# Kernel tuning notes

Hardware: AMD Instinct MI355X
Metric: run time of the kernel (lower is better)

## Reference

```python
import jax, jax.numpy as jnp
import numpy as np

N_HEAD = 16

def setup_inputs() -> dict:
    key = jax.random.key(0)
    ks = jax.random.split(key, 9)
    B, T, C = 2, 2048, 1024
    s = 0.02
    return {
        "x": jax.random.normal(ks[0], (B, T, C), dtype=jnp.float32),
        "Wk": jax.random.normal(ks[1], (C, C), dtype=jnp.float32) * s,
        "bk": jnp.zeros((C,), dtype=jnp.float32),
        "Wq": jax.random.normal(ks[2], (C, C), dtype=jnp.float32) * s,
        "bq": jnp.zeros((C,), dtype=jnp.float32),
        "Wv": jax.random.normal(ks[3], (C, C), dtype=jnp.float32) * s,
        "bv": jnp.zeros((C,), dtype=jnp.float32),
        "Wp": jax.random.normal(ks[4], (C, C), dtype=jnp.float32) * s,
        "bp": jnp.zeros((C,), dtype=jnp.float32),
    }

def reference(x, Wk, bk, Wq, bq, Wv, bv, Wp, bp):
    B, T, C = x.shape
    H = N_HEAD
    D = C // H
    # projections -> [B, H, T, D]
    def split_heads(y):
        return y.reshape(B, T, H, D).transpose(0, 2, 1, 3)
    k = split_heads(x @ Wk.T + bk)
    q = split_heads(x @ Wq.T + bq)
    v = split_heads(x @ Wv.T + bv)
    scale = 1.0 / jnp.sqrt(jnp.asarray(D, dtype=x.dtype))
    att = jnp.einsum("bhtd,bhsd->bhts", q, k) * scale  # [B,H,T,T]
    causal = jnp.tril(jnp.ones((T, T), dtype=bool))
    att = jnp.where(causal, att, jnp.asarray(-jnp.inf, dtype=att.dtype))
    att = jax.nn.softmax(att, axis=-1)
    y = jnp.einsum("bhts,bhsd->bhtd", att, v)  # [B,H,T,D]
    y = y.transpose(0, 2, 1, 3).reshape(B, T, C)
    return y @ Wp.T + bp
```

## Files before the change

### kernel.cpp

```cpp
#include <hip/hip_runtime.h>
#include <stdint.h>

typedef unsigned short u16;
typedef __attribute__((ext_vector_type(8))) short short8;
typedef __attribute__((ext_vector_type(4))) short short4v;
typedef __attribute__((ext_vector_type(4))) float float4v;

#define NB 2
#define NT 2048
#define NC 1024
#define NH 16
#define ND 64
#define NM (NB*NT)

#if defined(__has_builtin)
#if __has_builtin(__builtin_amdgcn_mfma_f32_16x16x16bf16_1k)
#define MFMA16(a, b, c) __builtin_amdgcn_mfma_f32_16x16x16bf16_1k(a, b, c, 0, 0, 0)
#endif
#endif
#ifndef MFMA16
static __device__ __forceinline__ float4v mfma16_asm(short4v a, short4v b, float4v c) {
  asm volatile("v_mfma_f32_16x16x16_bf16 %0, %1, %2, %0" : "+v"(c) : "v"(a), "v"(b));
  return c;
}
#define MFMA16(a, b, c) mfma16_asm(a, b, c)
#endif

#define WB4 asm volatile("s_waitcnt vmcnt(4)\n\ts_barrier" ::: "memory")
#define WB0 asm volatile("s_waitcnt vmcnt(0)\n\ts_barrier" ::: "memory")
#define BAR_PLAIN asm volatile("s_barrier" ::: "memory")

__device__ __forceinline__ u16 f2bf(float f) {
  union { float f; uint32_t u; } v; v.f = f;
  uint32_t u = v.u;
  u += 0x7fffu + ((u >> 16) & 1u);
  return (u16)(u >> 16);
}
__device__ __forceinline__ float bf2f(u16 u) {
  union { uint32_t u; float f; } v; v.u = ((uint32_t)u) << 16; return v.f;
}

__device__ __forceinline__ short4v pack4bf(float a, float b, float c, float d) {
  union { uint32_t u[2]; short4v s; } r;
  r.u[0] = __builtin_amdgcn_perm(__float_as_uint(b), __float_as_uint(a), 0x07060302u);
  r.u[1] = __builtin_amdgcn_perm(__float_as_uint(d), __float_as_uint(c), 0x07060302u);
  return r.s;
}

__device__ __forceinline__ void gld_lds16(const u16* g, u16* lds) {
  __builtin_amdgcn_global_load_lds(
      (const __attribute__((address_space(1))) uint32_t*)g,
      (__attribute__((address_space(3))) uint32_t*)lds,
      16, 0, 0);
}

__global__ __launch_bounds__(256) void cast_all(
    const float* __restrict__ x,  const float* __restrict__ wk,
    const float* __restrict__ wq, const float* __restrict__ wv,
    const float* __restrict__ wp,
    u16* __restrict__ xb, u16* __restrict__ wkb, u16* __restrict__ wqb,
    u16* __restrict__ wvb, u16* __restrict__ wpb) {
  const int NX = NM * NC / 4;
  const int NW = NC * NC / 4;
  int i = blockIdx.x * 256 + threadIdx.x;
  const float* src; u16* dst; int off;
  if (i < NX)            { src = x;  dst = xb;  off = i; }
  else if (i < NX+NW)    { src = wk; dst = wkb; off = i - NX; }
  else if (i < NX+2*NW)  { src = wq; dst = wqb; off = i - NX - NW; }
  else if (i < NX+3*NW)  { src = wv; dst = wvb; off = i - NX - 2*NW; }
  else if (i < NX+4*NW)  { src = wp; dst = wpb; off = i - NX - 3*NW; }
  else return;
  float4v f = ((const float4v*)src)[off];
  short4v o;
  o.x = (short)f2bf(f.x); o.y = (short)f2bf(f.y);
  o.z = (short)f2bf(f.z); o.w = (short)f2bf(f.w);
  ((short4v*)dst)[off] = o;
}

__device__ __forceinline__ void gemm_tile(
    const u16* __restrict__ A_tile, const u16* __restrict__ W_tile,
    u16* As, u16* Bs, float4v (&acc)[4][4]) {
  const int tid  = threadIdx.x;
  const int wave = tid >> 6, lane = tid & 63;
  const int quad = lane >> 4, l15 = lane & 15;
  const int wm = wave >> 1, wn = wave & 1;
  const int c8 = lane & 7, r8 = lane >> 3;

#pragma unroll
  for (int i = 0; i < 4; i++)
#pragma unroll
    for (int j = 0; j < 4; j++) acc[i][j] = (float4v){0.f, 0.f, 0.f, 0.f};

  for (int k0 = 0; k0 < NC; k0 += 64) {
#pragma unroll
    for (int i = 0; i < 4; i++) {
      int row = wave * 32 + i * 8 + r8;
      int gc  = c8 ^ (row & 7);
      gld_lds16(A_tile + row * NC + k0 + gc * 8, As + (wave * 32 + i * 8) * 64);
      gld_lds16(W_tile + row * NC + k0 + gc * 8, Bs + (wave * 32 + i * 8) * 64);
    }
    __syncthreads();
#pragma unroll
    for (int kk = 0; kk < 2; kk++) {
      short8 af[4], bf[4];
#pragma unroll
      for (int mt = 0; mt < 4; mt++) {
        int row = wm * 64 + mt * 16 + l15;
        int ch  = (kk * 4 + quad) ^ (row & 7);
        af[mt] = *(const short8*)(As + row * 64 + ch * 8);
      }
#pragma unroll
      for (int nt = 0; nt < 4; nt++) {
        int row = wn * 64 + nt * 16 + l15;
        int ch  = (kk * 4 + quad) ^ (row & 7);
        bf[nt] = *(const short8*)(Bs + row * 64 + ch * 8);
      }
#pragma unroll
      for (int mt = 0; mt < 4; mt++)
#pragma unroll
        for (int nt = 0; nt < 4; nt++)
          acc[mt][nt] = __builtin_amdgcn_mfma_f32_16x16x32_bf16(af[mt], bf[nt], acc[mt][nt], 0, 0, 0);
    }
    __syncthreads();
  }
}

__global__ __launch_bounds__(256) void qkv_gemm(
    const u16* __restrict__ xb,
    const u16* __restrict__ wqb, const u16* __restrict__ wkb, const u16* __restrict__ wvb,
    const float* __restrict__ bq, const float* __restrict__ bk, const float* __restrict__ bv,
    u16* __restrict__ Q, u16* __restrict__ K, u16* __restrict__ Vb) {
  __shared__ u16 As[128 * 64];
  __shared__ u16 Bs[128 * 64];
  const int id  = blockIdx.x;
  const int x8  = id & 7;
  const int rr  = id >> 3;
  const int mti = rr & 31;
  const int mat = rr >> 5;
  const int n0  = x8 * 128;
  const int m0  = mti * 128;
  const u16*   W    = (mat == 0) ? wqb : (mat == 1) ? wkb : wvb;
  const float* bias = (mat == 0) ? bq  : (mat == 1) ? bk  : bv;
  u16* dst = (mat == 0) ? Q : (mat == 1) ? K : Vb;
  const float osc = (mat == 0) ? 0.18033688f : 1.0f;

  float4v acc[4][4];
  gemm_tile(xb + m0 * NC, W + n0 * NC, As, Bs, acc);

  const int tid = threadIdx.x, wave = tid >> 6, lane = tid & 63;
  const int quad = lane >> 4, l15 = lane & 15;
  const int wm = wave >> 1, wn = wave & 1;
#pragma unroll
  for (int nt = 0; nt < 4; nt++) {
    int col = n0 + wn * 64 + nt * 16 + l15;
    float bval = bias[col];
#pragma unroll
    for (int mt = 0; mt < 4; mt++) {
      int rowb = m0 + wm * 64 + mt * 16 + quad * 4;
#pragma unroll
      for (int r = 0; r < 4; r++)
        dst[(size_t)(rowb + r) * NC + col] = f2bf((acc[mt][nt][r] + bval) * osc);
    }
  }
}

__global__ __launch_bounds__(256) void vtrans(const u16* __restrict__ V, u16* __restrict__ Vt) {
  __shared__ u16 tl[64 * 64];
  const int tid = threadIdx.x;
  const int bh = blockIdx.y, b = bh >> 4, h = bh & 15;
  const int t0 = blockIdx.x * 64;
#pragma unroll
  for (int it = 0; it < 2; it++) {
    int idx = it * 256 + tid;
    int row = idx >> 3;
    int ch  = idx & 7;
    short8 vv = *(const short8*)(V + (size_t)(b * NT + t0 + row) * NC + h * ND + ch * 8);
    int p   = ((row >> 2) & 3) * 16 + (row >> 4) * 4 + (row & 3);
    int off = ((p >> 3) ^ ch) * 8 + (p & 7);
#pragma unroll
    for (int j = 0; j < 8; j++) tl[(ch * 8 + j) * 64 + off] = (u16)vv[j];
  }
  __syncthreads();
#pragma unroll
  for (int it = 0; it < 2; it++) {
    int idx = it * 256 + tid;
    int d  = idx >> 3;
    int tc = idx & 7;
    short8 o = *(const short8*)(tl + d * 64 + ((tc ^ ((d >> 3) & 7)) << 3));
    *(short8*)(Vt + (size_t)(bh * ND + d) * NT + t0 + tc * 8) = o;
  }
}

__global__ __launch_bounds__(256, 4) void attn(
    const u16* __restrict__ Q, const u16* __restrict__ K,
    const u16* __restrict__ Vt, u16* __restrict__ O,
    u16* __restrict__ Opart, float* __restrict__ Lpart) {
  __shared__ u16 Kc[2][64 * 64];
  __shared__ u16 Vc[2][64 * 64];

  const int tid = threadIdx.x, wave = tid >> 6, lane = tid & 63;
  const int quad = lane >> 4, l15 = lane & 15;
  const int c8 = lane & 7, r8 = lane >> 3;
  const int id = blockIdx.x;
  const int rr = id >> 3;
  const int cls = rr % 30;
  const int bh = (id & 7) + 8 * (rr / 30);
  const int b = bh >> 4, h = bh & 15;

  int tile, k, c_lo, c_hi, sbase;
  if (cls < 6)        { tile = cls; k = 0;
                        c_lo = 0; c_hi = 2 * tile + 1; sbase = -1; }
  else if (cls < 18)  { tile = 6 + ((cls - 6) >> 1); k = (cls - 6) & 1;
                        int Ch = tile + 1;
                        c_lo = k * Ch; c_hi = c_lo + Ch - 1;
                        sbase = (tile - 6) * 2 + k; }
  else                { int d3 = cls - 18; int t3 = d3 / 3; k = d3 - 3 * t3;
                        tile = 12 + t3; int C = 2 * tile + 2;
                        c_lo = (k * C) / 3; c_hi = ((k + 1) * C) / 3 - 1;
                        sbase = 12 + t3 * 3 + k; }
  const bool partial = (sbase >= 0);
  const int qb0 = tile * 128 + wave * 32;

  short8 qf[2][2];
#pragma unroll
  for (int j = 0; j < 2; j++) {
    const u16* qrow = Q + (size_t)(b * NT + qb0 + j * 16 + l15) * NC + h * ND + quad * 8;
    qf[j][0] = *(const short8*)(qrow);
    qf[j][1] = *(const short8*)(qrow + 32);
  }

  float l_c[2] = {0.f, 0.f};
  float4v o_acc[2][4];
#pragma unroll
  for (int j = 0; j < 2; j++)
#pragma unroll
    for (int dt = 0; dt < 4; dt++) o_acc[j][dt] = (float4v){0.f, 0.f, 0.f, 0.f};

  int kOff[2], vOff[2], ldsOff[2];
#pragma unroll
  for (int ii = 0; ii < 2; ii++) {
    int row = wave * 16 + ii * 8 + r8;
    int gc  = c8 ^ (row & 7);
    kOff[ii]   = row * NC + gc * 8;
    vOff[ii]   = row * NT + gc * 8;
    ldsOff[ii] = (wave * 16 + ii * 8) * 64;
  }
  const u16* Kbase = K  + (size_t)b * NT * NC + h * ND;
  const u16* Vbase = Vt + (size_t)bh * ND * NT;

  auto stage = [&](int ci) {
    const int p = (ci - c_lo) & 1;
    const u16* kc = Kbase + (size_t)ci * (64 * NC);
    const u16* vc = Vbase + ci * 64;
#pragma unroll
    for (int ii = 0; ii < 2; ii++) {
      gld_lds16(kc + kOff[ii], Kc[p] + ldsOff[ii]);
      gld_lds16(vc + vOff[ii], Vc[p] + ldsOff[ii]);
    }
  };

  stage(c_lo);
  for (int i = c_lo; i <= c_hi; i++) {
    const int p = (i - c_lo) & 1;
    if (i < c_hi) { stage(i + 1); WB4; } else { WB0; }
    const u16* Ks = Kc[p];
    const u16* Vs = Vc[p];

    short4v pf[2][4];
#pragma unroll
    for (int sub = 0; sub < 4; sub++) {
      float4v a0 = (float4v){0.f, 0.f, 0.f, 0.f};
      float4v a1 = (float4v){0.f, 0.f, 0.f, 0.f};
#pragma unroll
      for (int kk = 0; kk < 2; kk++) {
        int row = sub * 16 + l15;
        int ch  = (kk * 4 + quad) ^ (row & 7);
        short8 kf = *(const short8*)(Ks + row * 64 + ch * 8);
        a0 = __builtin_amdgcn_mfma_f32_16x16x32_bf16(kf, qf[0][kk], a0, 0, 0, 0);
        a1 = __builtin_amdgcn_mfma_f32_16x16x32_bf16(kf, qf[1][kk], a1, 0, 0, 0);
      }
#pragma unroll
      for (int j = 0; j < 2; j++) {
        const float4v& a = (j == 0) ? a0 : a1;
        const bool mj = (i * 64 + 63) > (qb0 + j * 16);
        const int qg = qb0 + j * 16 + l15;
        float pv[4];
#pragma unroll
        for (int r = 0; r < 4; r++) {
          float pp = exp2f(a[r]);
          if (mj) {
            int sg = i * 64 + sub * 16 + quad * 4 + r;
            if (sg > qg) pp = 0.f;
          }
          pv[r] = pp;
        }
        l_c[j] += (pv[0] + pv[1]) + (pv[2] + pv[3]);
        pf[j][sub] = pack4bf(pv[0], pv[1], pv[2], pv[3]);
      }
    }

#pragma unroll
    for (int dt = 0; dt < 4; dt++) {
      int row = dt * 16 + l15;
      int swz = row & 7;
      short8 vA = *(const short8*)(Vs + row * 64 + ((2 * quad)     ^ swz) * 8);
      short8 vB = *(const short8*)(Vs + row * 64 + ((2 * quad + 1) ^ swz) * 8);
      short4v vA0 = __builtin_shufflevector(vA, vA, 0, 1, 2, 3);
      short4v vA1 = __builtin_shufflevector(vA, vA, 4, 5, 6, 7);
      short4v vB0 = __builtin_shufflevector(vB, vB, 0, 1, 2, 3);
      short4v vB1 = __builtin_shufflevector(vB, vB, 4, 5, 6, 7);
#pragma unroll
      for (int j = 0; j < 2; j++) {
        o_acc[j][dt] = MFMA16(vA0, pf[j][0], o_acc[j][dt]);
        o_acc[j][dt] = MFMA16(vA1, pf[j][1], o_acc[j][dt]);
        o_acc[j][dt] = MFMA16(vB0, pf[j][2], o_acc[j][dt]);
        o_acc[j][dt] = MFMA16(vB1, pf[j][3], o_acc[j][dt]);
      }
    }
    if (i < c_hi) BAR_PLAIN;
  }

  float l_tot[2];
#pragma unroll
  for (int j = 0; j < 2; j++) {
    float t = l_c[j];
    t += __shfl_xor(t, 16);
    t += __shfl_xor(t, 32);
    l_tot[j] = t;
  }

  if (!partial) {
#pragma unroll
    for (int j = 0; j < 2; j++) {
      float inv_l = 1.f / l_tot[j];
      const size_t orow = (size_t)(b * NT + qb0 + j * 16 + l15) * NC + h * ND;
#pragma unroll
      for (int dt = 0; dt < 4; dt++)
        *(short4v*)(O + orow + dt * 16 + quad * 4) =
            pack4bf(o_acc[j][dt][0] * inv_l, o_acc[j][dt][1] * inv_l,
                    o_acc[j][dt][2] * inv_l, o_acc[j][dt][3] * inv_l);
    }
  } else {
    const int slab = bh * 24 + sbase;
    u16* ob = Opart + (size_t)slab * 8192;
#pragma unroll
    for (int j = 0; j < 2; j++) {
      const int row = wave * 32 + j * 16 + l15;
#pragma unroll
      for (int dt = 0; dt < 4; dt++)
        *(short4v*)(ob + row * 64 + dt * 16 + quad * 4) =
            pack4bf(o_acc[j][dt][0], o_acc[j][dt][1],
                    o_acc[j][dt][2], o_acc[j][dt][3]);
      if (quad == 0)
        Lpart[slab * 128 + row] = l_tot[j];
    }
  }
}

__global__ __launch_bounds__(256) void combine(
    const u16* __restrict__ Opart, const float* __restrict__ Lp, u16* __restrict__ O) {
  int idx  = blockIdx.x * 256 + threadIdx.x;
  int tIdx = idx >> 13;
  int rem  = idx & 8191;
  int row  = rem >> 6, d = rem & 63;
  int bh   = tIdx / 10;
  int tt   = tIdx - bh * 10;
  int tile = 6 + tt;
  int S, sbase;
  if (tile < 12) { S = 2; sbase = (tile - 6) * 2; }
  else           { S = 3; sbase = 12 + (tile - 12) * 3; }
  int slab0 = bh * 24 + sbase;
  float osum = 0.f, lsum = 0.f;
  for (int s = 0; s < S; s++) {
    osum += bf2f(Opart[(size_t)(slab0 + s) * 8192 + rem]);
    lsum += Lp[(slab0 + s) * 128 + row];
  }
  int b = bh >> 4, h = bh & 15;
  int t = tile * 128 + row;
  O[(size_t)(b * NT + t) * NC + h * ND + d] = f2bf(osum / lsum);
}

__global__ __launch_bounds__(256) void out_gemm(
    const u16* __restrict__ Ob, const u16* __restrict__ wpb,
    const float* __restrict__ bp, float* __restrict__ out) {
  __shared__ u16 As[64 * 64];
  __shared__ u16 Bs[128 * 64];
  const int n0 = blockIdx.x * 128;
  const int m0 = blockIdx.y * 64;
  const int tid = threadIdx.x, wave = tid >> 6, lane = tid & 63;
  const int quad = lane >> 4, l15 = lane & 15;
  const int wm = wave >> 1, wn = wave & 1;
  const int c8 = lane & 7, r8 = lane >> 3;

  float4v acc[2][4];
#pragma unroll
  for (int i = 0; i < 2; i++)
#pragma unroll
    for (int j = 0; j < 4; j++) acc[i][j] = (float4v){0.f, 0.f, 0.f, 0.f};

  for (int k0 = 0; k0 < NC; k0 += 64) {
#pragma unroll
    for (int i = 0; i < 2; i++) {
      int row = wave * 16 + i * 8 + r8;
      int gc  = c8 ^ (row & 7);
      gld_lds16(Ob + (size_t)(m0 + row) * NC + k0 + gc * 8, As + (wave * 16 + i * 8) * 64);
    }
#pragma unroll
    for (int i = 0; i < 4; i++) {
      int row = wave * 32 + i * 8 + r8;
      int gc  = c8 ^ (row & 7);
      gld_lds16(wpb + (size_t)(n0 + row) * NC + k0 + gc * 8, Bs + (wave * 32 + i * 8) * 64);
    }
    __syncthreads();
#pragma unroll
    for (int kk = 0; kk < 2; kk++) {
      short8 af[2], bf[4];
#pragma unroll
      for (int mt = 0; mt < 2; mt++) {
        int row = wm * 32 + mt * 16 + l15;
        int ch  = (kk * 4 + quad) ^ (row & 7);
        af[mt] = *(const short8*)(As + row * 64 + ch * 8);
      }
#pragma unroll
      for (int nt = 0; nt < 4; nt++) {
        int row = wn * 64 + nt * 16 + l15;
        int ch  = (kk * 4 + quad) ^ (row & 7);
        bf[nt] = *(const short8*)(Bs + row * 64 + ch * 8);
      }
#pragma unroll
      for (int mt = 0; mt < 2; mt++)
#pragma unroll
        for (int nt = 0; nt < 4; nt++)
          acc[mt][nt] = __builtin_amdgcn_mfma_f32_16x16x32_bf16(af[mt], bf[nt], acc[mt][nt], 0, 0, 0);
    }
    __syncthreads();
  }

#pragma unroll
  for (int nt = 0; nt < 4; nt++) {
    int col = n0 + wn * 64 + nt * 16 + l15;
    float bval = bp[col];
#pragma unroll
    for (int mt = 0; mt < 2; mt++) {
      int rowb = m0 + wm * 32 + mt * 16 + quad * 4;
#pragma unroll
      for (int r = 0; r < 4; r++)
        out[(rowb + r) * NC + col] = acc[mt][nt][r] + bval;
    }
  }
}

extern "C" void kernel_launch(void* const* d_in, const int* in_sizes, int n_in,
                              void* d_out, int out_size, void* d_ws, size_t ws_size,
                              hipStream_t stream) {
  const float* x  = (const float*)d_in[0];
  const float* Wk = (const float*)d_in[1];
  const float* bk = (const float*)d_in[2];
  const float* Wq = (const float*)d_in[3];
  const float* bq = (const float*)d_in[4];
  const float* Wv = (const float*)d_in[5];
  const float* bv = (const float*)d_in[6];
  const float* Wp = (const float*)d_in[7];
  const float* bp = (const float*)d_in[8];
  float* out = (float*)d_out;

  uint8_t* ws = (uint8_t*)d_ws;
  const size_t MB = 1u << 20;
  u16* xb    = (u16*)(ws + 0 * MB);
  u16* wkb   = (u16*)(ws + 8 * MB);
  u16* wqb   = (u16*)(ws + 10 * MB);
  u16* wvb   = (u16*)(ws + 12 * MB);
  u16* wpb   = (u16*)(ws + 14 * MB);
  u16* Qb    = (u16*)(ws + 16 * MB);
  u16* Kb    = (u16*)(ws + 24 * MB);
  u16* Vtb   = (u16*)(ws + 32 * MB);
  u16* Vb    = (u16*)(ws + 40 * MB);
  u16* Ob    = (u16*)(ws + 40 * MB);
  u16* Opart = (u16*)(ws + 0 * MB);
  float* Lpart = (float*)(ws + 12 * MB);

  cast_all<<<8192, 256, 0, stream>>>(x, Wk, Wq, Wv, Wp, xb, wkb, wqb, wvb, wpb);
  qkv_gemm<<<768, 256, 0, stream>>>(xb, wqb, wkb, wvb, bq, bk, bv, Qb, Kb, Vb);
  vtrans<<<dim3(32, 32), 256, 0, stream>>>(Vb, Vtb);
  attn<<<960, 256, 0, stream>>>(Qb, Kb, Vtb, Ob, Opart, Lpart);
  combine<<<10240, 256, 0, stream>>>(Opart, Lpart, Ob);
  out_gemm<<<dim3(8, 64), 256, 0, stream>>>(Ob, wpb, bp, out);
}
```

Measured before the change: 210.1 us.

## Fuse V transpose into QKV GEMM epilogue and rebalance causal attention splits

For the V matrix, the QKV GEMM epilogue now writes its tile through shared memory in transposed order, straight into the Vt layout. This removes the separate vtrans kernel and the round trip of V through global memory. The causal attention work split is also reworked: 5 full tiles, 6 tiles split in two and 5 tiles split in three, giving 32 classes per group and 1024 blocks instead of 960. The partial-slab indexing, the combine grid and the Lpart offset are changed to match. The transposed epilogue adds an extra shared-memory pass and a barrier to the V-producing GEMM blocks.

```diff
diff --git a/kernel.cpp b/kernel.cpp
--- a/kernel.cpp
+++ b/kernel.cpp
@@ -129,9 +129,8 @@
     const u16* __restrict__ xb,
     const u16* __restrict__ wqb, const u16* __restrict__ wkb, const u16* __restrict__ wvb,
     const float* __restrict__ bq, const float* __restrict__ bk, const float* __restrict__ bv,
-    u16* __restrict__ Q, u16* __restrict__ K, u16* __restrict__ Vb) {
-  __shared__ u16 As[128 * 64];
-  __shared__ u16 Bs[128 * 64];
+    u16* __restrict__ Q, u16* __restrict__ K, u16* __restrict__ Vt) {
+  __shared__ u16 S[2][128 * 64];
   const int id  = blockIdx.x;
   const int x8  = id & 7;
   const int rr  = id >> 3;
@@ -141,53 +140,56 @@
   const int m0  = mti * 128;
   const u16*   W    = (mat == 0) ? wqb : (mat == 1) ? wkb : wvb;
   const float* bias = (mat == 0) ? bq  : (mat == 1) ? bk  : bv;
-  u16* dst = (mat == 0) ? Q : (mat == 1) ? K : Vb;
-  const float osc = (mat == 0) ? 0.18033688f : 1.0f;
 
   float4v acc[4][4];
-  gemm_tile(xb + m0 * NC, W + n0 * NC, As, Bs, acc);
+  gemm_tile(xb + m0 * NC, W + n0 * NC, S[0], S[1], acc);
 
   const int tid = threadIdx.x, wave = tid >> 6, lane = tid & 63;
   const int quad = lane >> 4, l15 = lane & 15;
   const int wm = wave >> 1, wn = wave & 1;
-#pragma unroll
-  for (int nt = 0; nt < 4; nt++) {
-    int col = n0 + wn * 64 + nt * 16 + l15;
-    float bval = bias[col];
-#pragma unroll
-    for (int mt = 0; mt < 4; mt++) {
-      int rowb = m0 + wm * 64 + mt * 16 + quad * 4;
-#pragma unroll
-      for (int r = 0; r < 4; r++)
-        dst[(size_t)(rowb + r) * NC + col] = f2bf((acc[mt][nt][r] + bval) * osc);
-    }
-  }
-}
-
-__global__ __launch_bounds__(256) void vtrans(const u16* __restrict__ V, u16* __restrict__ Vt) {
-  __shared__ u16 tl[64 * 64];
-  const int tid = threadIdx.x;
-  const int bh = blockIdx.y, b = bh >> 4, h = bh & 15;
-  const int t0 = blockIdx.x * 64;
-#pragma unroll
-  for (int it = 0; it < 2; it++) {
-    int idx = it * 256 + tid;
-    int row = idx >> 3;
-    int ch  = idx & 7;
-    short8 vv = *(const short8*)(V + (size_t)(b * NT + t0 + row) * NC + h * ND + ch * 8);
-    int p   = ((row >> 2) & 3) * 16 + (row >> 4) * 4 + (row & 3);
-    int off = ((p >> 3) ^ ch) * 8 + (p & 7);
-#pragma unroll
-    for (int j = 0; j < 8; j++) tl[(ch * 8 + j) * 64 + off] = (u16)vv[j];
-  }
-  __syncthreads();
-#pragma unroll
-  for (int it = 0; it < 2; it++) {
-    int idx = it * 256 + tid;
-    int d  = idx >> 3;
-    int tc = idx & 7;
-    short8 o = *(const short8*)(tl + d * 64 + ((tc ^ ((d >> 3) & 7)) << 3));
-    *(short8*)(Vt + (size_t)(bh * ND + d) * NT + t0 + tc * 8) = o;
+
+  if (mat != 2) {
+    u16* dst = (mat == 0) ? Q : K;
+    const float osc = (mat == 0) ? 0.18033688f : 1.0f;
+#pragma unroll
+    for (int nt = 0; nt < 4; nt++) {
+      int col = n0 + wn * 64 + nt * 16 + l15;
+      float bval = bias[col];
+#pragma unroll
+      for (int mt = 0; mt < 4; mt++) {
+        int rowb = m0 + wm * 64 + mt * 16 + quad * 4;
+#pragma unroll
+        for (int r = 0; r < 4; r++)
+          dst[(size_t)(rowb + r) * NC + col] = f2bf((acc[mt][nt][r] + bval) * osc);
+      }
+    }
+  } else {
+    u16* tile = (u16*)S;
+#pragma unroll
+    for (int nt = 0; nt < 4; nt++) {
+      int c = wn * 64 + nt * 16 + l15;
+      float bval = bias[n0 + c];
+#pragma unroll
+      for (int mt = 0; mt < 4; mt++) {
+#pragma unroll
+        for (int r = 0; r < 4; r++) {
+          int mr  = mt * 4 + r;
+          int off = wm * 64 + quad * 16 + mr;
+          int ck  = (off >> 3) ^ (c & 15);
+          tile[c * 128 + ck * 8 + (off & 7)] = f2bf(acc[mt][nt][r] + bval);
+        }
+      }
+    }
+    __syncthreads();
+    const int b  = m0 >> 11, t0 = m0 & 2047;
+    const int bh0 = b * NH + (n0 >> 6);
+#pragma unroll
+    for (int it = 0; it < 8; it++) {
+      int idx = it * 256 + tid;
+      int c = idx >> 4, ck = idx & 15;
+      short8 v = *(const short8*)(tile + c * 128 + ((ck ^ (c & 15)) * 8));
+      *(short8*)(Vt + ((size_t)(bh0 + (c >> 6)) * ND + (c & 63)) * NT + t0 + ck * 8) = v;
+    }
   }
 }
 
@@ -203,19 +205,19 @@
   const int c8 = lane & 7, r8 = lane >> 3;
   const int id = blockIdx.x;
   const int rr = id >> 3;
-  const int cls = rr % 30;
-  const int bh = (id & 7) + 8 * (rr / 30);
+  const int cls = rr & 31;
+  const int bh = (id & 7) + 8 * (rr >> 5);
   const int b = bh >> 4, h = bh & 15;
 
   int tile, k, c_lo, c_hi, sbase;
-  if (cls < 6)        { tile = cls; k = 0;
+  if (cls < 5)        { tile = cls;
                         c_lo = 0; c_hi = 2 * tile + 1; sbase = -1; }
-  else if (cls < 18)  { tile = 6 + ((cls - 6) >> 1); k = (cls - 6) & 1;
-                        int Ch = tile + 1;
-                        c_lo = k * Ch; c_hi = c_lo + Ch - 1;
-                        sbase = (tile - 6) * 2 + k; }
-  else                { int d3 = cls - 18; int t3 = d3 / 3; k = d3 - 3 * t3;
-                        tile = 12 + t3; int C = 2 * tile + 2;
+  else if (cls < 17)  { tile = 5 + ((cls - 5) >> 1); k = (cls - 5) & 1;
+                        int half = tile + 1;
+                        c_lo = k * half; c_hi = c_lo + half - 1;
+                        sbase = (tile - 5) * 2 + k; }
+  else                { int d3 = cls - 17; int t3 = d3 / 3; k = d3 - 3 * t3;
+                        tile = 11 + t3; int C = 2 * tile + 2;
                         c_lo = (k * C) / 3; c_hi = ((k + 1) * C) / 3 - 1;
                         sbase = 12 + t3 * 3 + k; }
   const bool partial = (sbase >= 0);
@@ -341,7 +343,7 @@
                     o_acc[j][dt][2] * inv_l, o_acc[j][dt][3] * inv_l);
     }
   } else {
-    const int slab = bh * 24 + sbase;
+    const int slab = bh * 27 + sbase;
     u16* ob = Opart + (size_t)slab * 8192;
 #pragma unroll
     for (int j = 0; j < 2; j++) {
@@ -363,13 +365,13 @@
   int tIdx = idx >> 13;
   int rem  = idx & 8191;
   int row  = rem >> 6, d = rem & 63;
-  int bh   = tIdx / 10;
-  int tt   = tIdx - bh * 10;
-  int tile = 6 + tt;
-  int S, sbase;
-  if (tile < 12) { S = 2; sbase = (tile - 6) * 2; }
-  else           { S = 3; sbase = 12 + (tile - 12) * 3; }
-  int slab0 = bh * 24 + sbase;
+  int bh   = tIdx / 11;
+  int tt   = tIdx - bh * 11;
+  int tile = 5 + tt;
+  int S, sb;
+  if (tile < 11) { S = 2; sb = (tile - 5) * 2; }
+  else           { S = 3; sb = 12 + (tile - 11) * 3; }
+  int slab0 = bh * 27 + sb;
   float osum = 0.f, lsum = 0.f;
   for (int s = 0; s < S; s++) {
     osum += bf2f(Opart[(size_t)(slab0 + s) * 8192 + rem]);
@@ -474,15 +476,13 @@
   u16* Qb    = (u16*)(ws + 16 * MB);
   u16* Kb    = (u16*)(ws + 24 * MB);
   u16* Vtb   = (u16*)(ws + 32 * MB);
-  u16* Vb    = (u16*)(ws + 40 * MB);
   u16* Ob    = (u16*)(ws + 40 * MB);
   u16* Opart = (u16*)(ws + 0 * MB);
-  float* Lpart = (float*)(ws + 12 * MB);
+  float* Lpart = (float*)(ws + 13 * MB + 512 * 1024);
 
   cast_all<<<8192, 256, 0, stream>>>(x, Wk, Wq, Wv, Wp, xb, wkb, wqb, wvb, wpb);
-  qkv_gemm<<<768, 256, 0, stream>>>(xb, wqb, wkb, wvb, bq, bk, bv, Qb, Kb, Vb);
-  vtrans<<<dim3(32, 32), 256, 0, stream>>>(Vb, Vtb);
-  attn<<<960, 256, 0, stream>>>(Qb, Kb, Vtb, Ob, Opart, Lpart);
-  combine<<<10240, 256, 0, stream>>>(Opart, Lpart, Ob);
+  qkv_gemm<<<768, 256, 0, stream>>>(xb, wqb, wkb, wvb, bq, bk, bv, Qb, Kb, Vtb);
+  attn<<<1024, 256, 0, stream>>>(Qb, Kb, Vtb, Ob, Opart, Lpart);
+  combine<<<11264, 256, 0, stream>>>(Opart, Lpart, Ob);
   out_gemm<<<dim3(8, 64), 256, 0, stream>>>(Ob, wpb, bp, out);
 }
```

Result: slower. 224.7 us (+7.0%).
